# Optimization experiments

Hardware: AMD Instinct MI355X
Metric: run time of the kernel (lower is better)

The kernel has to match this reference:

```python
import jax, jax.numpy as jnp
import numpy as np

B, T, D = 32, 1024, 1024
N, L = 77, 768
H = 8
TED = 2048  # time_embed_dim
EPS = 1e-5


def _ln(x, g, b):
    m = jnp.mean(x, axis=-1, keepdims=True)
    v = jnp.var(x, axis=-1, keepdims=True)
    return (x - m) * jax.lax.rsqrt(v + EPS) * g + b


def setup_inputs() -> dict:
    key = jax.random.key(0)
    ks = jax.random.split(key, 16)
    s = lambda fan_in: 1.0 / np.sqrt(fan_in)
    return {
        "x": jax.random.normal(ks[0], (B, T, D), jnp.float32),
        "xf": jax.random.normal(ks[1], (B, N, L), jnp.float32),
        "emb": jax.random.normal(ks[2], (B, TED), jnp.float32),
        "norm_g": jnp.ones((D,), jnp.float32),
        "norm_b": jnp.zeros((D,), jnp.float32),
        "tnorm_g": jnp.ones((L,), jnp.float32),
        "tnorm_b": jnp.zeros((L,), jnp.float32),
        "Wq": jax.random.normal(ks[3], (D, D), jnp.float32) * s(D),
        "bq": jnp.zeros((D,), jnp.float32),
        "Wk": jax.random.normal(ks[4], (L, D), jnp.float32) * s(L),
        "bk": jnp.zeros((D,), jnp.float32),
        "Wv": jax.random.normal(ks[5], (L, D), jnp.float32) * s(L),
        "bv": jnp.zeros((D,), jnp.float32),
        "emb_W": jax.random.normal(ks[6], (TED, 2 * D), jnp.float32) * s(TED),
        "emb_b": jnp.zeros((2 * D,), jnp.float32),
        "onorm_g": jnp.ones((D,), jnp.float32),
        "onorm_b": jnp.zeros((D,), jnp.float32),
        "Wo": jax.random.normal(ks[7], (D, D), jnp.float32) * s(D),
        "bo": jnp.zeros((D,), jnp.float32),
    }


def reference(x, xf, emb, norm_g, norm_b, tnorm_g, tnorm_b, Wq, bq, Wk, bk, Wv, bv,
              emb_W, emb_b, onorm_g, onorm_b, Wo, bo):
    Bc, Tc, Dc = x.shape
    Nc = xf.shape[1]
    hd = Dc // H
    # projections
    q = _ln(x, norm_g, norm_b) @ Wq + bq                      # [B,T,D]
    xfn = _ln(xf, tnorm_g, tnorm_b)                           # [B,N,L]
    k = (xfn @ Wk + bk).reshape(Bc, Nc, H, hd)                # [B,N,H,hd]
    v = (xfn @ Wv + bv).reshape(Bc, Nc, H, hd)                # [B,N,H,hd]
    q = jax.nn.softmax(q.reshape(Bc, Tc, H, hd), axis=-1)     # softmax over head_dim
    k = jax.nn.softmax(k, axis=1)                             # softmax over N (key tokens)
    # linear-attention: no TxN matrix
    attn = jnp.einsum('bnhd,bnhl->bhdl', k, v)                # [B,H,hd,hd]
    y = jnp.einsum('bthd,bhdl->bthl', q, attn).reshape(Bc, Tc, Dc)
    # StylizationBlock
    emb_out = jax.nn.silu(emb) @ emb_W + emb_b                # [B,2D]
    scale, shift = jnp.split(emb_out[:, None, :], 2, axis=2)  # [B,1,D] each
    h = _ln(y, onorm_g, onorm_b) * (1.0 + scale) + shift
    h = jax.nn.silu(h) @ Wo + bo
    return x + h
```

## Files before the change

kernel.cpp:

```cpp
#include <hip/hip_runtime.h>
#include <hip/hip_bf16.h>
#include <math.h>

namespace {

constexpr int Bc  = 32;
constexpr int Tc  = 1024;
constexpr int Dc  = 1024;
constexpr int Nt  = 77;
constexpr int Lc  = 768;
constexpr int HDc = 128;
constexpr int TEDc = 2048;
constexpr float EPSc = 1e-5f;

typedef __attribute__((ext_vector_type(8))) short bf16x8;
typedef __attribute__((ext_vector_type(8))) unsigned short u16x8;
typedef __attribute__((ext_vector_type(4))) float f32x4;

__device__ __forceinline__ float silu_f(float x) { return x / (1.f + __expf(-x)); }

__device__ __forceinline__ unsigned short f2bf(float f) {
  unsigned u = __float_as_uint(f);
  return (unsigned short)((u + 0x7fffu + ((u >> 16) & 1u)) >> 16);
}
__device__ __forceinline__ float bf2f(unsigned short h) {
  return __uint_as_float(((unsigned)h) << 16);
}

__device__ __forceinline__ void gload16(const void* g, void* l) {
  __builtin_amdgcn_global_load_lds((const __attribute__((address_space(1))) void*)g,
                                   (__attribute__((address_space(3))) void*)l, 16, 0, 0);
}

__device__ __forceinline__ int rowswz(int r) {
  return (((r >> 3) & 1) << 1) | ((r >> 1) & 1);
}

__global__ __launch_bounds__(256) void ln_bf16_kernel(
    const float* __restrict__ src, unsigned short* __restrict__ dst, int cols,
    const float* __restrict__ g, const float* __restrict__ b)
{
  const int row = blockIdx.x;
  const float* p = src + (size_t)row * cols;
  const int c = threadIdx.x * 4;
  float4 v = make_float4(0.f, 0.f, 0.f, 0.f);
  if (c < cols) v = *reinterpret_cast<const float4*>(p + c);
  float s  = v.x + v.y + v.z + v.w;
  float sq = v.x * v.x + v.y * v.y + v.z * v.z + v.w * v.w;
  __shared__ float red[2][4];
  __shared__ float mr[2];
  for (int o = 32; o > 0; o >>= 1) { s += __shfl_down(s, o); sq += __shfl_down(sq, o); }
  const int wid = threadIdx.x >> 6, lane = threadIdx.x & 63;
  if (lane == 0) { red[0][wid] = s; red[1][wid] = sq; }
  __syncthreads();
  if (threadIdx.x == 0) {
    const float S  = red[0][0] + red[0][1] + red[0][2] + red[0][3];
    const float SQ = red[1][0] + red[1][1] + red[1][2] + red[1][3];
    const float mean = S / cols;
    const float var  = SQ / cols - mean * mean;
    mr[0] = mean; mr[1] = rsqrtf(var + EPSc);
  }
  __syncthreads();
  if (c < cols) {
    const float mean = mr[0], rstd = mr[1];
    ushort4 o;
    o.x = f2bf((v.x - mean) * rstd * g[c + 0] + b[c + 0]);
    o.y = f2bf((v.y - mean) * rstd * g[c + 1] + b[c + 1]);
    o.z = f2bf((v.z - mean) * rstd * g[c + 2] + b[c + 2]);
    o.w = f2bf((v.w - mean) * rstd * g[c + 3] + b[c + 3]);
    *reinterpret_cast<ushort4*>(dst + (size_t)row * cols + c) = o;
  }
}

__global__ __launch_bounds__(256) void convT_bf16_kernel(
    const float* __restrict__ W, unsigned short* __restrict__ Wt, int K, int N)
{
  __shared__ float t[32][33];
  const int n0 = blockIdx.x * 32, k0 = blockIdx.y * 32;
  const int tx = threadIdx.x & 31, ty = threadIdx.x >> 5;
  #pragma unroll
  for (int dy = 0; dy < 32; dy += 8)
    t[ty + dy][tx] = W[(size_t)(k0 + ty + dy) * N + n0 + tx];
  __syncthreads();
  #pragma unroll
  for (int dy = 0; dy < 32; dy += 8)
    Wt[(size_t)(n0 + ty + dy) * K + k0 + tx] = f2bf(t[tx][ty + dy]);
}

__global__ __launch_bounds__(256) void convT2_bf16_kernel(
    const float* __restrict__ W0, unsigned short* __restrict__ T0,
    const float* __restrict__ W1, unsigned short* __restrict__ T1, int K, int N)
{
  __shared__ float t[32][33];
  const float* W = blockIdx.z ? W1 : W0;
  unsigned short* Wt = blockIdx.z ? T1 : T0;
  const int n0 = blockIdx.x * 32, k0 = blockIdx.y * 32;
  const int tx = threadIdx.x & 31, ty = threadIdx.x >> 5;
  #pragma unroll
  for (int dy = 0; dy < 32; dy += 8)
    t[ty + dy][tx] = W[(size_t)(k0 + ty + dy) * N + n0 + tx];
  __syncthreads();
  #pragma unroll
  for (int dy = 0; dy < 32; dy += 8)
    Wt[(size_t)(n0 + ty + dy) * K + k0 + tx] = f2bf(t[tx][ty + dy]);
}

template<int EPI, int NT>
__global__ __launch_bounds__(512, 4) void gemm2_kernel(
    const unsigned short* __restrict__ A, const unsigned short* __restrict__ Bt,
    const float* __restrict__ bias, const float* __restrict__ bias2, int bsplit,
    void* __restrict__ Cout, int M, int N, const float* __restrict__ xres)
{
  constexpr int K = NT * 32;
  __shared__ unsigned short lds[36864];
  const int tid = threadIdx.x, wid = tid >> 6, lane = tid & 63;
  const int ntx = N >> 7;
  int swz = blockIdx.x;
  const int nwg = gridDim.x;
  if ((nwg & 7) == 0) { const int cpx = nwg >> 3; swz = (swz & 7) * cpx + (swz >> 3); }
  const int bx = swz % ntx, by = swz / ntx;
  const int bm0 = by << 8, bn0 = bx << 7;
  const int wr = wid >> 1, wc = wid & 1, lhi = lane >> 4, llo = lane & 15;

  const int srow = lane >> 2;
  const int scol = (((lane & 3) ^ rowswz(srow)) * 8);
  int ar0 = bm0 + wid * 32 + srow;      if (ar0 >= M) ar0 = M - 1;
  int ar1 = bm0 + wid * 32 + 16 + srow; if (ar1 >= M) ar1 = M - 1;
  const int br = bn0 + wid * 16 + srow;
  const unsigned short* Ag0 = A  + (size_t)ar0 * K + scol;
  const unsigned short* Ag1 = A  + (size_t)ar1 * K + scol;
  const unsigned short* Bg  = Bt + (size_t)br  * K + scol;
  const int alc0 = (wid * 2) * 512, alc1 = (wid * 2 + 1) * 512, blc = wid * 512;
  const int rx = rowswz(llo);
  const int aoff = wr * 2048 + llo * 32 + ((lhi ^ rx) * 8);
  const int boff = wc * 2048 + llo * 32 + ((lhi ^ rx) * 8);

  f32x4 acc[4][4] = {};

  gload16(Ag0,      &lds[alc0]);
  gload16(Ag1,      &lds[alc1]);
  gload16(Bg,       &lds[24576 + blc]);
  gload16(Ag0 + 32, &lds[8192 + alc0]);
  gload16(Ag1 + 32, &lds[8192 + alc1]);
  gload16(Bg  + 32, &lds[24576 + 4096 + blc]);

  for (int t = 0; t < NT; t += 3) {
    #pragma unroll
    for (int j = 0; j < 3; j++) {
      const int tt = t + j;
      if (tt < NT) {
        if (tt + 2 < NT) {
          const int k2 = (tt + 2) << 5;
          constexpr int PB0 = 2, PB1 = 0, PB2 = 1;
          const int pb = (j == 0) ? PB0 : (j == 1) ? PB1 : PB2;
          gload16(Ag0 + k2, &lds[pb * 8192 + alc0]);
          gload16(Ag1 + k2, &lds[pb * 8192 + alc1]);
          gload16(Bg  + k2, &lds[24576 + pb * 4096 + blc]);
          asm volatile("s_waitcnt vmcnt(6)" ::: "memory");
        } else if (tt + 1 < NT) {
          asm volatile("s_waitcnt vmcnt(3)" ::: "memory");
        } else {
          asm volatile("s_waitcnt vmcnt(0)" ::: "memory");
        }
        __builtin_amdgcn_s_barrier();
        bf16x8 a_[4], b_[4];
        #pragma unroll
        for (int mi = 0; mi < 4; mi++)
          a_[mi] = *(const bf16x8*)(&lds[j * 8192 + aoff + mi * 512]);
        #pragma unroll
        for (int ni = 0; ni < 4; ni++)
          b_[ni] = *(const bf16x8*)(&lds[24576 + j * 4096 + boff + ni * 512]);
        __builtin_amdgcn_s_setprio(1);
        #pragma unroll
        for (int mi = 0; mi < 4; mi++)
          #pragma unroll
          for (int ni = 0; ni < 4; ni++)
            acc[mi][ni] = __builtin_amdgcn_mfma_f32_16x16x32_bf16(a_[mi], b_[ni], acc[mi][ni], 0, 0, 0);
        __builtin_amdgcn_s_setprio(0);
        __builtin_amdgcn_s_barrier();
      }
    }
  }

  if constexpr (EPI != 2) {
    #pragma unroll
    for (int mi = 0; mi < 4; mi++) {
      #pragma unroll
      for (int ni = 0; ni < 4; ni++) {
        const int col = bn0 + wc * 64 + ni * 16 + llo;
        const float bs = (bsplit > 0 && col >= bsplit) ? bias2[col - bsplit] : bias[col];
        #pragma unroll
        for (int r = 0; r < 4; r++) {
          const int row = bm0 + wr * 64 + mi * 16 + lhi * 4 + r;
          if (row < M) {
            float v = acc[mi][ni][r] + bs;
            if (EPI == 1) v += xres[(size_t)row * N + col];
            ((float*)Cout)[(size_t)row * N + col] = v;
          }
        }
      }
    }
  } else {
    __syncthreads();
    #pragma unroll
    for (int mi = 0; mi < 4; mi++) {
      #pragma unroll
      for (int ni = 0; ni < 4; ni++) {
        const int col = wc * 64 + ni * 16 + llo;
        const float bs = bias[bn0 + col];
        #pragma unroll
        for (int r = 0; r < 4; r++) {
          const int row = wr * 64 + mi * 16 + lhi * 4 + r;
          lds[row * 128 + (col ^ ((row & 7) << 3))] = f2bf(acc[mi][ni][r] + bs);
        }
      }
    }
    __syncthreads();
    const int row = tid >> 1, cb = (tid & 1) * 64;
    const int sw = (row & 7) << 3;
    float mx = -1e30f;
    #pragma unroll
    for (int g = 0; g < 8; g++) {
      u16x8 u = *(const u16x8*)(&lds[row * 128 + ((cb + g * 8) ^ sw)]);
      #pragma unroll
      for (int j = 0; j < 8; j++) mx = fmaxf(mx, bf2f(u[j]));
    }
    mx = fmaxf(mx, __shfl_xor(mx, 1));
    float ssum = 0.f;
    #pragma unroll
    for (int g = 0; g < 8; g++) {
      unsigned short* p = &lds[row * 128 + ((cb + g * 8) ^ sw)];
      u16x8 u = *(const u16x8*)p;
      u16x8 e;
      #pragma unroll
      for (int j = 0; j < 8; j++) {
        float ev = __expf(bf2f(u[j]) - mx);
        ssum += ev;
        e[j] = f2bf(ev);
      }
      *(u16x8*)p = e;
    }
    ssum += __shfl_xor(ssum, 1);
    const float inv = 1.f / ssum;
    unsigned short* Cb = (unsigned short*)Cout;
    #pragma unroll
    for (int g = 0; g < 8; g++) {
      u16x8 u = *(const u16x8*)(&lds[row * 128 + ((cb + g * 8) ^ sw)]);
      u16x8 o;
      #pragma unroll
      for (int j = 0; j < 8; j++) o[j] = f2bf(bf2f(u[j]) * inv);
      *(u16x8*)(&Cb[(size_t)(bm0 + row) * N + bn0 + cb + g * 8]) = o;
    }
  }
}

__global__ __launch_bounds__(256) void attn_fused_kernel(
    const float* __restrict__ kv, unsigned short* __restrict__ attnT) {
  const int bh = blockIdx.x;
  const int b = bh >> 3, h = bh & 7;
  __shared__ float ks[Nt][HDc];
  __shared__ float vs[Nt][HDc];
  const float* kb = kv + (size_t)b * Nt * 2048 + h * HDc;
  const float* vb = kv + (size_t)b * Nt * 2048 + 1024 + h * HDc;
  for (int i = threadIdx.x; i < Nt * HDc; i += 256) {
    const int n = i >> 7, d = i & 127;
    ks[n][d] = kb[(size_t)n * 2048 + d];
    vs[n][d] = vb[(size_t)n * 2048 + d];
  }
  __syncthreads();
  if (threadIdx.x < HDc) {
    const int d = threadIdx.x;
    float m = -1e30f;
    for (int n = 0; n < Nt; n++) m = fmaxf(m, ks[n][d]);
    float s = 0.f;
    for (int n = 0; n < Nt; n++) { float e = __expf(ks[n][d] - m); ks[n][d] = e; s += e; }
    const float inv = 1.f / s;
    for (int n = 0; n < Nt; n++) ks[n][d] *= inv;
  }
  __syncthreads();
  const int tx = threadIdx.x & 15, ty = threadIdx.x >> 4;
  float acc[8][8] = {};
  for (int n = 0; n < Nt; n++) {
    float a[8], w[8];
    #pragma unroll
    for (int i = 0; i < 8; i++) a[i] = vs[n][ty + 16 * i];
    #pragma unroll
    for (int j = 0; j < 8; j++) w[j] = ks[n][tx + 16 * j];
    #pragma unroll
    for (int i = 0; i < 8; i++)
      #pragma unroll
      for (int j = 0; j < 8; j++)
        acc[i][j] += a[i] * w[j];
  }
  unsigned short* ab = attnT + (size_t)bh * HDc * HDc;
  #pragma unroll
  for (int i = 0; i < 8; i++)
    #pragma unroll
    for (int j = 0; j < 8; j++)
      ab[(size_t)(ty + 16 * i) * HDc + tx + 16 * j] = f2bf(acc[i][j]);
}

__global__ __launch_bounds__(256) void y_mfma_kernel(
    unsigned short* __restrict__ q, const unsigned short* __restrict__ attnT)
{
  __shared__ unsigned short lds[16384];
  const int tid = threadIdx.x, wid = tid >> 6, lane = tid & 63;
  const int bh = blockIdx.y, b = bh >> 3, h = bh & 7;
  const int bm0 = blockIdx.x << 7;
  const int wr = wid >> 1, wc = wid & 1, lhi = lane >> 4, llo = lane & 15;

  unsigned short* Abase = q + ((size_t)b * Tc) * Dc + h * HDc;
  const unsigned short* Btb = attnT + (size_t)bh * HDc * HDc;

  const int srow = lane >> 2, scol = (lane & 3) * 8;
  const int ar0 = bm0 + wid * 32 + srow, ar1 = ar0 + 16;
  const int br0 = wid * 32 + srow,       br1 = br0 + 16;
  const unsigned short* Ag0 = Abase + (size_t)ar0 * Dc + scol;
  const unsigned short* Ag1 = Abase + (size_t)ar1 * Dc + scol;
  const unsigned short* Bg0 = Btb + (size_t)br0 * HDc + scol;
  const unsigned short* Bg1 = Btb + (size_t)br1 * HDc + scol;
  const int lc0 = (wid * 2 + 0) * 512, lc1 = (wid * 2 + 1) * 512;
  const int aoff = wr * 2048 + llo * 32 + lhi * 8;
  const int boff = wc * 2048 + llo * 32 + lhi * 8;

  f32x4 acc[4][4] = {};

  gload16(Ag0, &lds[lc0]);
  gload16(Ag1, &lds[lc1]);
  gload16(Bg0, &lds[8192 + lc0]);
  gload16(Bg1, &lds[8192 + lc1]);
  __syncthreads();

  int cur = 0;
  for (int t = 1; t < 4; ++t) {
    const int nb = cur ^ 1;
    const int k0 = t << 5;
    gload16(Ag0 + k0, &lds[nb * 4096 + lc0]);
    gload16(Ag1 + k0, &lds[nb * 4096 + lc1]);
    gload16(Bg0 + k0, &lds[8192 + nb * 4096 + lc0]);
    gload16(Bg1 + k0, &lds[8192 + nb * 4096 + lc1]);
    bf16x8 a_[4], b_[4];
    #pragma unroll
    for (int mi = 0; mi < 4; mi++) a_[mi] = *(const bf16x8*)(&lds[cur * 4096 + aoff + mi * 512]);
    #pragma unroll
    for (int ni = 0; ni < 4; ni++) b_[ni] = *(const bf16x8*)(&lds[8192 + cur * 4096 + boff + ni * 512]);
    #pragma unroll
    for (int mi = 0; mi < 4; mi++)
      #pragma unroll
      for (int ni = 0; ni < 4; ni++)
        acc[mi][ni] = __builtin_amdgcn_mfma_f32_16x16x32_bf16(a_[mi], b_[ni], acc[mi][ni], 0, 0, 0);
    __syncthreads();
    cur = nb;
  }
  {
    bf16x8 a_[4], b_[4];
    #pragma unroll
    for (int mi = 0; mi < 4; mi++) a_[mi] = *(const bf16x8*)(&lds[cur * 4096 + aoff + mi * 512]);
    #pragma unroll
    for (int ni = 0; ni < 4; ni++) b_[ni] = *(const bf16x8*)(&lds[8192 + cur * 4096 + boff + ni * 512]);
    #pragma unroll
    for (int mi = 0; mi < 4; mi++)
      #pragma unroll
      for (int ni = 0; ni < 4; ni++)
        acc[mi][ni] = __builtin_amdgcn_mfma_f32_16x16x32_bf16(a_[mi], b_[ni], acc[mi][ni], 0, 0, 0);
  }

  __syncthreads();
  #pragma unroll
  for (int mi = 0; mi < 4; mi++) {
    #pragma unroll
    for (int ni = 0; ni < 4; ni++) {
      const int col = wc * 64 + ni * 16 + llo;
      #pragma unroll
      for (int r = 0; r < 4; r++) {
        const int row = wr * 64 + mi * 16 + lhi * 4 + r;
        lds[row * 128 + (col ^ ((row & 7) << 3))] = f2bf(acc[mi][ni][r]);
      }
    }
  }
  __syncthreads();
  const int row = tid >> 1, cb = (tid & 1) * 64;
  const int sw = (row & 7) << 3;
  #pragma unroll
  for (int g = 0; g < 8; g++) {
    u16x8 u = *(const u16x8*)(&lds[row * 128 + ((cb + g * 8) ^ sw)]);
    *(u16x8*)(&Abase[(size_t)(bm0 + row) * Dc + cb + g * 8]) = u;
  }
}

__global__ __launch_bounds__(256) void ln_mod_silu_bf16_kernel(
    unsigned short* __restrict__ y, const float* __restrict__ ss,
    const float* __restrict__ g, const float* __restrict__ bvec) {
  const int row = blockIdx.x;
  const int b = row >> 10;
  unsigned short* p = y + (size_t)row * Dc;
  const int c = threadIdx.x * 4;
  ushort4 u = *reinterpret_cast<const ushort4*>(p + c);
  float vv[4] = {bf2f(u.x), bf2f(u.y), bf2f(u.z), bf2f(u.w)};
  float s  = vv[0] + vv[1] + vv[2] + vv[3];
  float sq = vv[0]*vv[0] + vv[1]*vv[1] + vv[2]*vv[2] + vv[3]*vv[3];
  __shared__ float red[2][4];
  __shared__ float mr[2];
  for (int o = 32; o > 0; o >>= 1) { s += __shfl_down(s, o); sq += __shfl_down(sq, o); }
  const int wid = threadIdx.x >> 6, lane = threadIdx.x & 63;
  if (lane == 0) { red[0][wid] = s; red[1][wid] = sq; }
  __syncthreads();
  if (threadIdx.x == 0) {
    const float S  = red[0][0] + red[0][1] + red[0][2] + red[0][3];
    const float SQ = red[1][0] + red[1][1] + red[1][2] + red[1][3];
    const float mean = S / Dc;
    const float var = SQ / Dc - mean * mean;
    mr[0] = mean; mr[1] = rsqrtf(var + EPSc);
  }
  __syncthreads();
  const float mean = mr[0], rstd = mr[1];
  const float* ssb = ss + (size_t)b * 2 * Dc;
  ushort4 o;
  float t0 = (vv[0] - mean) * rstd * g[c + 0] + bvec[c + 0];
  float t1 = (vv[1] - mean) * rstd * g[c + 1] + bvec[c + 1];
  float t2 = (vv[2] - mean) * rstd * g[c + 2] + bvec[c + 2];
  float t3 = (vv[3] - mean) * rstd * g[c + 3] + bvec[c + 3];
  o.x = f2bf(silu_f(t0 * (1.f + ssb[c + 0]) + ssb[Dc + c + 0]));
  o.y = f2bf(silu_f(t1 * (1.f + ssb[c + 1]) + ssb[Dc + c + 1]));
  o.z = f2bf(silu_f(t2 * (1.f + ssb[c + 2]) + ssb[Dc + c + 2]));
  o.w = f2bf(silu_f(t3 * (1.f + ssb[c + 3]) + ssb[Dc + c + 3]));
  *reinterpret_cast<ushort4*>(p + c) = o;
}

__global__ __launch_bounds__(256) void silu_emb_kernel(
    const float* __restrict__ emb, float* __restrict__ sile) {
  const int i = (blockIdx.x * 256 + threadIdx.x) * 4;
  float4 v = *reinterpret_cast<const float4*>(emb + i);
  v.x = silu_f(v.x); v.y = silu_f(v.y); v.z = silu_f(v.z); v.w = silu_f(v.w);
  *reinterpret_cast<float4*>(sile + i) = v;
}

__global__ __launch_bounds__(256) void emb_part_kernel(
    const float* __restrict__ sile, const float* __restrict__ W,
    float* __restrict__ part) {
  const int split = blockIdx.y;
  const int n = blockIdx.x * 256 + threadIdx.x;
  const int k0 = split * 64;
  const float* se = sile + k0;
  const float* Wp = W + (size_t)k0 * (2 * Dc) + n;
  float acc[32] = {};
  for (int kk = 0; kk < 64; kk++) {
    const float w = Wp[(size_t)kk * (2 * Dc)];
    #pragma unroll
    for (int m = 0; m < 32; m++)
      acc[m] = fmaf(se[m * TEDc + kk], w, acc[m]);
  }
  float* pp = part + (size_t)split * 32 * (2 * Dc) + n;
  #pragma unroll
  for (int m = 0; m < 32; m++) pp[(size_t)m * (2 * Dc)] = acc[m];
}

__global__ __launch_bounds__(256) void emb_reduce_kernel(
    const float* __restrict__ part, const float* __restrict__ bias,
    float* __restrict__ ssb) {
  const int i = blockIdx.x * 256 + threadIdx.x;
  const int n = i & (2 * Dc - 1);
  float s = bias[n];
  #pragma unroll 8
  for (int sp = 0; sp < 32; sp++) s += part[(size_t)sp * 32 * (2 * Dc) + i];
  ssb[i] = s;
}

}

extern "C" void kernel_launch(void* const* d_in, const int* in_sizes, int n_in,
                              void* d_out, int out_size, void* d_ws, size_t ws_size,
                              hipStream_t stream) {
  const float* x       = (const float*)d_in[0];
  const float* xf      = (const float*)d_in[1];
  const float* emb     = (const float*)d_in[2];
  const float* norm_g  = (const float*)d_in[3];
  const float* norm_b  = (const float*)d_in[4];
  const float* tnorm_g = (const float*)d_in[5];
  const float* tnorm_b = (const float*)d_in[6];
  const float* Wq      = (const float*)d_in[7];
  const float* bq      = (const float*)d_in[8];
  const float* Wk      = (const float*)d_in[9];
  const float* bk      = (const float*)d_in[10];
  const float* Wv      = (const float*)d_in[11];
  const float* bv_     = (const float*)d_in[12];
  const float* emb_W   = (const float*)d_in[13];
  const float* emb_b   = (const float*)d_in[14];
  const float* onorm_g = (const float*)d_in[15];
  const float* onorm_b = (const float*)d_in[16];
  const float* Wo      = (const float*)d_in[17];
  const float* bo      = (const float*)d_in[18];
  float* out = (float*)d_out;

  char* ws = (char*)d_ws;
  unsigned short* Ab = (unsigned short*)ws;
  char* R = ws;
  unsigned short* qb   = (unsigned short*)(ws + 67108864);
  unsigned short* Wq_t = (unsigned short*)(ws + 134217728);
  unsigned short* Wk_t = (unsigned short*)(ws + 136314880);
  unsigned short* Wv_t = (unsigned short*)(ws + 137887744);
  unsigned short* Wo_t = (unsigned short*)(ws + 139460608);
  float*          ssb  = (float*)(ws + 141557760);
  float*          sile = (float*)(ws + 141819904);
  float*          part = (float*)(ws + 142082048);
  unsigned short* xfb   = (unsigned short*)(R);
  float*          kv    = (float*)(R + 3784704);
  unsigned short* attnT = (unsigned short*)(R + 23969792);

  const int Mq  = Bc * Tc;
  const int Mkv = Bc * Nt;

  ln_bf16_kernel<<<Mq, 256, 0, stream>>>(x, Ab, Dc, norm_g, norm_b);
  convT_bf16_kernel<<<dim3(Dc / 32, Dc / 32), 256, 0, stream>>>(Wq, Wq_t, Dc, Dc);
  convT2_bf16_kernel<<<dim3(Dc / 32, Lc / 32, 2), 256, 0, stream>>>(Wk, Wk_t, Wv, Wv_t, Lc, Dc);
  convT_bf16_kernel<<<dim3(Dc / 32, Dc / 32), 256, 0, stream>>>(Wo, Wo_t, Dc, Dc);

  gemm2_kernel<2, 32><<<(Dc / 128) * (Mq / 256), 512, 0, stream>>>(
      Ab, Wq_t, bq, nullptr, 0, qb, Mq, Dc, nullptr);

  ln_bf16_kernel<<<Mkv, 256, 0, stream>>>(xf, xfb, Lc, tnorm_g, tnorm_b);
  gemm2_kernel<0, 24><<<(2048 / 128) * ((Mkv + 255) / 256), 512, 0, stream>>>(
      xfb, Wk_t, bk, bv_, 1024, kv, Mkv, 2048, nullptr);
  attn_fused_kernel<<<Bc * 8, 256, 0, stream>>>(kv, attnT);

  silu_emb_kernel<<<(Bc * TEDc) / 1024, 256, 0, stream>>>(emb, sile);
  emb_part_kernel<<<dim3(8, 32), 256, 0, stream>>>(sile, emb_W, part);
  emb_reduce_kernel<<<(Bc * 2 * Dc) / 256, 256, 0, stream>>>(part, emb_b, ssb);

  y_mfma_kernel<<<dim3(Tc / 128, Bc * 8), 256, 0, stream>>>(qb, attnT);
  ln_mod_silu_bf16_kernel<<<Mq, 256, 0, stream>>>(qb, ssb, onorm_g, onorm_b);
  gemm2_kernel<1, 32><<<(Dc / 128) * (Mq / 256), 512, 0, stream>>>(
      qb, Wo_t, bo, nullptr, 0, out, Mq, Dc, x);
}
```

Measured before the change: 467.4 us.

## Fuse per-head y MFMA with output LayerNorm, modulation and SiLU

Replaces the separate y = q·attn MFMA kernel and the LayerNorm/modulate/SiLU kernel with one kernel. Each block covers 32 rows across all 8 heads, one head per wave, so the full 1024-wide row statistics can be reduced in LDS without writing the intermediate y. This removes one full bf16 write-and-read round trip of the B×T×D activation and one launch. In exchange, operands are loaded directly from global memory with no LDS staging, each block holds 64KB of LDS and runs at low occupancy (launch bounds 512,1), and y is no longer rounded to bf16 before the LayerNorm.

```diff
diff --git a/kernel.cpp b/kernel.cpp
--- a/kernel.cpp
+++ b/kernel.cpp
@@ -300,131 +300,107 @@
       ab[(size_t)(ty + 16 * i) * HDc + tx + 16 * j] = f2bf(acc[i][j]);
 }
 
-__global__ __launch_bounds__(256) void y_mfma_kernel(
-    unsigned short* __restrict__ q, const unsigned short* __restrict__ attnT)
+__global__ __launch_bounds__(512, 1) void y_ln_fused_kernel(
+    unsigned short* __restrict__ q, const unsigned short* __restrict__ attnT,
+    const float* __restrict__ ss, const float* __restrict__ g,
+    const float* __restrict__ bvec)
 {
-  __shared__ unsigned short lds[16384];
-  const int tid = threadIdx.x, wid = tid >> 6, lane = tid & 63;
-  const int bh = blockIdx.y, b = bh >> 3, h = bh & 7;
-  const int bm0 = blockIdx.x << 7;
-  const int wr = wid >> 1, wc = wid & 1, lhi = lane >> 4, llo = lane & 15;
-
-  unsigned short* Abase = q + ((size_t)b * Tc) * Dc + h * HDc;
-  const unsigned short* Btb = attnT + (size_t)bh * HDc * HDc;
-
-  const int srow = lane >> 2, scol = (lane & 3) * 8;
-  const int ar0 = bm0 + wid * 32 + srow, ar1 = ar0 + 16;
-  const int br0 = wid * 32 + srow,       br1 = br0 + 16;
-  const unsigned short* Ag0 = Abase + (size_t)ar0 * Dc + scol;
-  const unsigned short* Ag1 = Abase + (size_t)ar1 * Dc + scol;
-  const unsigned short* Bg0 = Btb + (size_t)br0 * HDc + scol;
-  const unsigned short* Bg1 = Btb + (size_t)br1 * HDc + scol;
-  const int lc0 = (wid * 2 + 0) * 512, lc1 = (wid * 2 + 1) * 512;
-  const int aoff = wr * 2048 + llo * 32 + lhi * 8;
-  const int boff = wc * 2048 + llo * 32 + lhi * 8;
-
-  f32x4 acc[4][4] = {};
-
-  gload16(Ag0, &lds[lc0]);
-  gload16(Ag1, &lds[lc1]);
-  gload16(Bg0, &lds[8192 + lc0]);
-  gload16(Bg1, &lds[8192 + lc1]);
-  __syncthreads();
-
-  int cur = 0;
-  for (int t = 1; t < 4; ++t) {
-    const int nb = cur ^ 1;
-    const int k0 = t << 5;
-    gload16(Ag0 + k0, &lds[nb * 4096 + lc0]);
-    gload16(Ag1 + k0, &lds[nb * 4096 + lc1]);
-    gload16(Bg0 + k0, &lds[8192 + nb * 4096 + lc0]);
-    gload16(Bg1 + k0, &lds[8192 + nb * 4096 + lc1]);
-    bf16x8 a_[4], b_[4];
-    #pragma unroll
-    for (int mi = 0; mi < 4; mi++) a_[mi] = *(const bf16x8*)(&lds[cur * 4096 + aoff + mi * 512]);
-    #pragma unroll
-    for (int ni = 0; ni < 4; ni++) b_[ni] = *(const bf16x8*)(&lds[8192 + cur * 4096 + boff + ni * 512]);
-    #pragma unroll
-    for (int mi = 0; mi < 4; mi++)
-      #pragma unroll
-      for (int ni = 0; ni < 4; ni++)
-        acc[mi][ni] = __builtin_amdgcn_mfma_f32_16x16x32_bf16(a_[mi], b_[ni], acc[mi][ni], 0, 0, 0);
-    __syncthreads();
-    cur = nb;
-  }
-  {
-    bf16x8 a_[4], b_[4];
-    #pragma unroll
-    for (int mi = 0; mi < 4; mi++) a_[mi] = *(const bf16x8*)(&lds[cur * 4096 + aoff + mi * 512]);
-    #pragma unroll
-    for (int ni = 0; ni < 4; ni++) b_[ni] = *(const bf16x8*)(&lds[8192 + cur * 4096 + boff + ni * 512]);
-    #pragma unroll
-    for (int mi = 0; mi < 4; mi++)
-      #pragma unroll
-      for (int ni = 0; ni < 4; ni++)
-        acc[mi][ni] = __builtin_amdgcn_mfma_f32_16x16x32_bf16(a_[mi], b_[ni], acc[mi][ni], 0, 0, 0);
-  }
-
-  __syncthreads();
-  #pragma unroll
-  for (int mi = 0; mi < 4; mi++) {
-    #pragma unroll
-    for (int ni = 0; ni < 4; ni++) {
-      const int col = wc * 64 + ni * 16 + llo;
+  __shared__ unsigned short olds[32 * 1024];
+  __shared__ float stats[32][8][2];
+  __shared__ float mrs[32][2];
+  const int tid = threadIdx.x, h = tid >> 6, lane = tid & 63;
+  const int lhi = lane >> 4, llo = lane & 15;
+  const int b = blockIdx.y;
+  const int row0 = blockIdx.x << 5;
+  unsigned short* qbase = q + ((size_t)(b * Tc + row0)) * Dc;
+  const unsigned short* at = attnT + (size_t)(b * 8 + h) * HDc * HDc;
+
+  bf16x8 a_[2][4];
+  #pragma unroll
+  for (int mi = 0; mi < 2; mi++)
+    #pragma unroll
+    for (int kk = 0; kk < 4; kk++)
+      a_[mi][kk] = *(const bf16x8*)(qbase + (size_t)(mi * 16 + llo) * Dc + h * HDc + kk * 32 + lhi * 8);
+
+  f32x4 acc[2][8] = {};
+  #pragma unroll
+  for (int ni = 0; ni < 8; ni++) {
+    bf16x8 b_[4];
+    #pragma unroll
+    for (int kk = 0; kk < 4; kk++)
+      b_[kk] = *(const bf16x8*)(at + (size_t)(ni * 16 + llo) * HDc + kk * 32 + lhi * 8);
+    #pragma unroll
+    for (int kk = 0; kk < 4; kk++) {
+      acc[0][ni] = __builtin_amdgcn_mfma_f32_16x16x32_bf16(a_[0][kk], b_[kk], acc[0][ni], 0, 0, 0);
+      acc[1][ni] = __builtin_amdgcn_mfma_f32_16x16x32_bf16(a_[1][kk], b_[kk], acc[1][ni], 0, 0, 0);
+    }
+  }
+
+  float ps[2][4], pq[2][4];
+  #pragma unroll
+  for (int mi = 0; mi < 2; mi++)
+    #pragma unroll
+    for (int r = 0; r < 4; r++) {
+      float s = 0.f, sq = 0.f;
+      #pragma unroll
+      for (int ni = 0; ni < 8; ni++) { float v = acc[mi][ni][r]; s += v; sq += v * v; }
+      ps[mi][r] = s; pq[mi][r] = sq;
+    }
+  #pragma unroll
+  for (int o = 1; o < 16; o <<= 1) {
+    #pragma unroll
+    for (int mi = 0; mi < 2; mi++)
       #pragma unroll
       for (int r = 0; r < 4; r++) {
-        const int row = wr * 64 + mi * 16 + lhi * 4 + r;
-        lds[row * 128 + (col ^ ((row & 7) << 3))] = f2bf(acc[mi][ni][r]);
-      }
-    }
-  }
-  __syncthreads();
-  const int row = tid >> 1, cb = (tid & 1) * 64;
-  const int sw = (row & 7) << 3;
-  #pragma unroll
-  for (int g = 0; g < 8; g++) {
-    u16x8 u = *(const u16x8*)(&lds[row * 128 + ((cb + g * 8) ^ sw)]);
-    *(u16x8*)(&Abase[(size_t)(bm0 + row) * Dc + cb + g * 8]) = u;
-  }
-}
-
-__global__ __launch_bounds__(256) void ln_mod_silu_bf16_kernel(
-    unsigned short* __restrict__ y, const float* __restrict__ ss,
-    const float* __restrict__ g, const float* __restrict__ bvec) {
-  const int row = blockIdx.x;
-  const int b = row >> 10;
-  unsigned short* p = y + (size_t)row * Dc;
-  const int c = threadIdx.x * 4;
-  ushort4 u = *reinterpret_cast<const ushort4*>(p + c);
-  float vv[4] = {bf2f(u.x), bf2f(u.y), bf2f(u.z), bf2f(u.w)};
-  float s  = vv[0] + vv[1] + vv[2] + vv[3];
-  float sq = vv[0]*vv[0] + vv[1]*vv[1] + vv[2]*vv[2] + vv[3]*vv[3];
-  __shared__ float red[2][4];
-  __shared__ float mr[2];
-  for (int o = 32; o > 0; o >>= 1) { s += __shfl_down(s, o); sq += __shfl_down(sq, o); }
-  const int wid = threadIdx.x >> 6, lane = threadIdx.x & 63;
-  if (lane == 0) { red[0][wid] = s; red[1][wid] = sq; }
-  __syncthreads();
-  if (threadIdx.x == 0) {
-    const float S  = red[0][0] + red[0][1] + red[0][2] + red[0][3];
-    const float SQ = red[1][0] + red[1][1] + red[1][2] + red[1][3];
-    const float mean = S / Dc;
-    const float var = SQ / Dc - mean * mean;
-    mr[0] = mean; mr[1] = rsqrtf(var + EPSc);
-  }
-  __syncthreads();
-  const float mean = mr[0], rstd = mr[1];
-  const float* ssb = ss + (size_t)b * 2 * Dc;
-  ushort4 o;
-  float t0 = (vv[0] - mean) * rstd * g[c + 0] + bvec[c + 0];
-  float t1 = (vv[1] - mean) * rstd * g[c + 1] + bvec[c + 1];
-  float t2 = (vv[2] - mean) * rstd * g[c + 2] + bvec[c + 2];
-  float t3 = (vv[3] - mean) * rstd * g[c + 3] + bvec[c + 3];
-  o.x = f2bf(silu_f(t0 * (1.f + ssb[c + 0]) + ssb[Dc + c + 0]));
-  o.y = f2bf(silu_f(t1 * (1.f + ssb[c + 1]) + ssb[Dc + c + 1]));
-  o.z = f2bf(silu_f(t2 * (1.f + ssb[c + 2]) + ssb[Dc + c + 2]));
-  o.w = f2bf(silu_f(t3 * (1.f + ssb[c + 3]) + ssb[Dc + c + 3]));
-  *reinterpret_cast<ushort4*>(p + c) = o;
+        ps[mi][r] += __shfl_xor(ps[mi][r], o);
+        pq[mi][r] += __shfl_xor(pq[mi][r], o);
+      }
+  }
+  if (llo == 0) {
+    #pragma unroll
+    for (int mi = 0; mi < 2; mi++)
+      #pragma unroll
+      for (int r = 0; r < 4; r++) {
+        const int row = mi * 16 + lhi * 4 + r;
+        stats[row][h][0] = ps[mi][r];
+        stats[row][h][1] = pq[mi][r];
+      }
+  }
+  __syncthreads();
+  if (tid < 32) {
+    float S = 0.f, Q = 0.f;
+    #pragma unroll
+    for (int w = 0; w < 8; w++) { S += stats[tid][w][0]; Q += stats[tid][w][1]; }
+    const float mean = S / 1024.f;
+    const float var = Q / 1024.f - mean * mean;
+    mrs[tid][0] = mean; mrs[tid][1] = rsqrtf(var + EPSc);
+  }
+  __syncthreads();
+
+  const float* ssb = ss + (size_t)b * 2048;
+  #pragma unroll
+  for (int ni = 0; ni < 8; ni++) {
+    const int col = h * 128 + ni * 16 + llo;
+    const float gg = g[col], bb = bvec[col];
+    const float sc = 1.f + ssb[col], sh = ssb[1024 + col];
+    #pragma unroll
+    for (int mi = 0; mi < 2; mi++)
+      #pragma unroll
+      for (int r = 0; r < 4; r++) {
+        const int row = mi * 16 + lhi * 4 + r;
+        float v = (acc[mi][ni][r] - mrs[row][0]) * mrs[row][1] * gg + bb;
+        v = v * sc + sh;
+        olds[row * 1024 + (col ^ ((row & 7) << 3))] = f2bf(silu_f(v));
+      }
+  }
+  __syncthreads();
+  const int orow = tid & 31, och = tid >> 5;
+  const int osw = (orow & 7) << 3;
+  #pragma unroll
+  for (int g2 = 0; g2 < 8; g2++) {
+    u16x8 u = *(const u16x8*)(&olds[orow * 1024 + ((och * 64 + g2 * 8) ^ osw)]);
+    *(u16x8*)(qbase + (size_t)orow * Dc + och * 64 + g2 * 8) = u;
+  }
 }
 
 __global__ __launch_bounds__(256) void silu_emb_kernel(
@@ -527,8 +503,8 @@
   emb_part_kernel<<<dim3(8, 32), 256, 0, stream>>>(sile, emb_W, part);
   emb_reduce_kernel<<<(Bc * 2 * Dc) / 256, 256, 0, stream>>>(part, emb_b, ssb);
 
-  y_mfma_kernel<<<dim3(Tc / 128, Bc * 8), 256, 0, stream>>>(qb, attnT);
-  ln_mod_silu_bf16_kernel<<<Mq, 256, 0, stream>>>(qb, ssb, onorm_g, onorm_b);
+  y_ln_fused_kernel<<<dim3(Tc / 32, Bc), 512, 0, stream>>>(qb, attnT, ssb, onorm_g, onorm_b);
+
   gemm2_kernel<1, 32><<<(Dc / 128) * (Mq / 256), 512, 0, stream>>>(
       qb, Wo_t, bo, nullptr, 0, out, Mq, Dc, x);
 }
```

Result: slower. 490.7 us (+5.0%).
